# Kernel optimization log

Measured on AMD Instinct MI355X. Metric: run time of the kernel, lower is better.

## Reference

```python
import jax, jax.numpy as jnp
import numpy as np

N_WIRES = 8
DIM = 2 ** N_WIRES  # 256 amplitudes
# PauliZ sign table: Z_SIGNS[w, i] = +1 if bit w of basis index i is 0 else -1
_bits = (np.arange(DIM)[None, :] >> (N_WIRES - 1 - np.arange(N_WIRES))[:, None]) & 1
Z_SIGNS = jnp.asarray(1.0 - 2.0 * _bits, dtype=jnp.float32)  # [8, 256]


def quantum_project(t, theta):
    """Batched 8-wire circuit: RX(x_w) encoder + trainable RX(theta_w) (RX gates on the
    same wire compose additively), then CNOT ring, then <Z_w> for each wire.
    t: [B, S, E] -> returns [B, S, H, 8]."""
    B, S, E = t.shape
    H = E // N_WIRES
    ang = (t.reshape(B, S, H, N_WIRES) + theta) * 0.5  # RX(a)RX(b)=RX(a+b)
    q0 = jnp.cos(ang).astype(jnp.complex64)
    q1 = (-1j * jnp.sin(ang)).astype(jnp.complex64)
    # Build product state |psi> = \otimes_w [cos(a_w/2), -i sin(a_w/2)] -> [B,S,H,256]
    state = jnp.ones((B, S, H, 1), jnp.complex64)
    for w in range(N_WIRES):
        qb = jnp.stack([q0[..., w], q1[..., w]], axis=-1)  # [B,S,H,2]
        state = (state[..., :, None] * qb[..., None, :]).reshape(B, S, H, -1)
    state = state.reshape((B, S, H) + (2,) * N_WIRES)  # wire w on axis 3+w
    # CNOT chain 0->1,...,6->7 then ring-closing 7->0
    for cw, tw in [(w, w + 1) for w in range(N_WIRES - 1)] + [(N_WIRES - 1, 0)]:
        s0 = jax.lax.index_in_dim(state, 0, axis=3 + cw, keepdims=True)
        s1 = jnp.flip(jax.lax.index_in_dim(state, 1, axis=3 + cw, keepdims=True), axis=3 + tw)
        state = jnp.concatenate([s0, s1], axis=3 + cw)
    amps = state.reshape(B, S, H, DIM)
    probs = amps.real * amps.real + amps.imag * amps.imag  # [B,S,H,256] float32
    return jnp.einsum('bshd,wd->bshw', probs, Z_SIGNS)  # <Z_w> per wire


def setup_inputs() -> dict:
    key = jax.random.key(0)
    kx, kq, kk, kv, ko, kt = jax.random.split(key, 6)
    B, S, E = 16, 512, 64
    scale = 1.0 / np.sqrt(E)
    return {
        'x': jax.random.normal(kx, (B, S, E), dtype=jnp.float32),
        'Wq': jax.random.normal(kq, (E, E), dtype=jnp.float32) * scale,
        'Wk': jax.random.normal(kk, (E, E), dtype=jnp.float32) * scale,
        'Wv': jax.random.normal(kv, (E, E), dtype=jnp.float32) * scale,
        'Wo': jax.random.normal(ko, (E, E), dtype=jnp.float32) * scale,
        'theta': jax.random.uniform(kt, (N_WIRES,), dtype=jnp.float32, minval=0.0, maxval=2.0 * np.pi),
    }


def reference(x, Wq, Wk, Wv, Wo, theta):
    B, S, E = x.shape
    q = quantum_project(x @ Wq.T, theta)  # [B,S,H,8]
    k = quantum_project(x @ Wk.T, theta)
    v = quantum_project(x @ Wv.T, theta)
    # NOTE: original code never transposes heads to dim 1, so attention mixes HEADS
    # per token: scores [B,S,H,H]. Faithfully reproduced. d_k = 8.
    scores = jnp.einsum('bsiw,bsjw->bsij', q, k) / jnp.float32(np.sqrt(N_WIRES))
    attn = jax.nn.softmax(scores, axis=-1)  # dropout is identity in eval
    out = jnp.einsum('bsij,bsjw->bsiw', attn, v)  # [B,S,H,8]
    # original: out.transpose(1,2).contiguous().view(B,-1,E) -> scrambled layout
    out = out.transpose(0, 2, 1, 3).reshape(B, -1, E)
    return out @ Wo.T
```

## Files before the change

kernel.cpp:

```cpp
#include <hip/hip_runtime.h>


typedef float  f32x4  __attribute__((ext_vector_type(4)));
typedef short  bf16x8 __attribute__((ext_vector_type(8)));
typedef unsigned short u16;
typedef unsigned int   u32;

#define WRS 72
#define SPS 68

#define DPP_SHR_STEP(d, j, sh)                                                 \
    {                                                                          \
        float _t = __int_as_float(__builtin_amdgcn_update_dpp(                 \
            0x3f800000, __float_as_int(d), 0x110 + sh, 0xf, 0xf, false));      \
        d *= ((j) >= (sh)) ? _t : 1.0f;                                        \
    }

__device__ __forceinline__ u32 bfh(float f) {
    const u32 u = __float_as_uint(f);
    return (u + 0x7FFFu + ((u >> 16) & 1u)) >> 16;
}
__device__ __forceinline__ void bfsplit(float f, u32& h, u32& l) {
    h = bfh(f);
    l = bfh(f - __uint_as_float(h << 16));
}

#define MFMA3(acc, ah, al, bh, bl)                                             \
    acc = __builtin_amdgcn_mfma_f32_16x16x32_bf16(al, bh, acc, 0, 0, 0);       \
    acc = __builtin_amdgcn_mfma_f32_16x16x32_bf16(ah, bl, acc, 0, 0, 0);       \
    acc = __builtin_amdgcn_mfma_f32_16x16x32_bf16(ah, bh, acc, 0, 0, 0);

__global__ __launch_bounds__(512, 1)
void qattn_fused(const float* __restrict__ xg,
                 const float* __restrict__ wqg, const float* __restrict__ wkg,
                 const float* __restrict__ wvg, const float* __restrict__ wog,
                 const float* __restrict__ thg,
                 float* __restrict__ outg)
{
    __shared__ u16 sWh[4 * 64 * WRS];
    __shared__ u16 sWl[4 * 64 * WRS];
    __shared__ u16 sXh[32 * WRS];
    __shared__ u16 sXl[32 * WRS];
    __shared__ __align__(16) float sP[96 * SPS];
    __shared__ u16 sSh[32 * WRS];
    __shared__ u16 sSl[32 * WRS];

    const int tid  = threadIdx.x;
    const int lane = tid & 63;
    const int wg   = tid >> 6;
    const int l15  = lane & 15;
    const int quad = lane >> 4;
    const int j    = lane & 7;
    const int b    = blockIdx.x >> 4;
    const int grp  = blockIdx.x & 15;

    {
        const float* gm[4] = {wqg, wkg, wvg, wog};
        #pragma unroll
        for (int r = 0; r < 8; ++r) {
            const int m   = r >> 1;
            const int idx = (r & 1) * 512 + tid;
            const float4 v = ((const float4*)gm[m])[idx];
            const int e = idx >> 4, c = idx & 15;
            u32 h0, l0, h1, l1, h2, l2, h3, l3;
            bfsplit(v.x, h0, l0); bfsplit(v.y, h1, l1);
            bfsplit(v.z, h2, l2); bfsplit(v.w, h3, l3);
            const int o = (m * 64 + e) * WRS + 4 * c;
            *(uint2*)&sWh[o] = make_uint2(h0 | (h1 << 16), h2 | (h3 << 16));
            *(uint2*)&sWl[o] = make_uint2(l0 | (l1 << 16), l2 | (l3 << 16));
        }
    }
    {
        const float4 v = ((const float4*)(xg + (size_t)(b * 512 + grp * 32) * 64))[tid];
        const int t = tid >> 4, c = tid & 15;
        u32 h0, l0, h1, l1, h2, l2, h3, l3;
        bfsplit(v.x, h0, l0); bfsplit(v.y, h1, l1);
        bfsplit(v.z, h2, l2); bfsplit(v.w, h3, l3);
        const int o = t * WRS + 4 * c;
        *(uint2*)&sXh[o] = make_uint2(h0 | (h1 << 16), h2 | (h3 << 16));
        *(uint2*)&sXl[o] = make_uint2(l0 | (l1 << 16), l2 | (l3 << 16));
    }
    const float thf = thg[j];
    __syncthreads();

    #pragma unroll
    for (int ia = 0; ia < 3; ++ia) {
        const int aid = wg * 3 + ia;
        const int mt = aid & 1, nt = (aid >> 1) & 3, m = aid >> 3;
        const int arow = (mt * 16 + l15) * WRS + quad * 8;
        const int brow = (m * 64 + nt * 16 + l15) * WRS + quad * 8;
        const bf16x8 ah0 = *(const bf16x8*)&sXh[arow];
        const bf16x8 ah1 = *(const bf16x8*)&sXh[arow + 32];
        const bf16x8 al0 = *(const bf16x8*)&sXl[arow];
        const bf16x8 al1 = *(const bf16x8*)&sXl[arow + 32];
        const bf16x8 bh0 = *(const bf16x8*)&sWh[brow];
        const bf16x8 bh1 = *(const bf16x8*)&sWh[brow + 32];
        const bf16x8 bl0 = *(const bf16x8*)&sWl[brow];
        const bf16x8 bl1 = *(const bf16x8*)&sWl[brow + 32];
        f32x4 acc = {0.f, 0.f, 0.f, 0.f};
        MFMA3(acc, ah0, al0, bh0, bl0)
        MFMA3(acc, ah1, al1, bh1, bl1)
        #pragma unroll
        for (int r = 0; r < 4; ++r) {
            const float c = __cosf(acc[r] + thf);
            float d = c;
            DPP_SHR_STEP(d, j, 1)
            DPP_SHR_STEP(d, j, 2)
            DPP_SHR_STEP(d, j, 4)
            float ex = (j == 0) ? 1.0f : c;
            DPP_SHR_STEP(ex, j, 1)
            DPP_SHR_STEP(ex, j, 2)
            DPP_SHR_STEP(ex, j, 4)
            const int row  = m * 32 + mt * 16 + quad * 4 + r;
            const int base = row * SPS + nt * 16 + l15;
            if (j > 0)  sP[base]     = d;
            if (j == 7) sP[base - 7] = ex;
        }
    }
    __syncthreads();

    if (wg < 4) {
        const int tg = wg * 8 + (lane >> 3);
        const int i  = j;
        const int qb = tg * SPS;
        const int kb = (32 + tg) * SPS;
        const int vb = (64 + tg) * SPS;
        float q[8];
        *(float4*)&q[0] = *(const float4*)&sP[qb + 8 * i];
        *(float4*)&q[4] = *(const float4*)&sP[qb + 8 * i + 4];
        float pr[8];
        float sum = 0.f;
        #pragma unroll
        for (int jj = 0; jj < 8; ++jj) {
            const float4 k0 = *(const float4*)&sP[kb + 8 * jj];
            const float4 k1 = *(const float4*)&sP[kb + 8 * jj + 4];
            float s = q[0] * k0.x;
            s = fmaf(q[1], k0.y, s); s = fmaf(q[2], k0.z, s);
            s = fmaf(q[3], k0.w, s); s = fmaf(q[4], k1.x, s);
            s = fmaf(q[5], k1.y, s); s = fmaf(q[6], k1.z, s);
            s = fmaf(q[7], k1.w, s);
            pr[jj] = __expf(s * 0.35355339059327373f);
            sum += pr[jj];
        }
        const float rinv = 1.0f / sum;
        float o[8];
        #pragma unroll
        for (int w = 0; w < 8; ++w) o[w] = 0.f;
        #pragma unroll
        for (int jj = 0; jj < 8; ++jj) {
            const float4 v0 = *(const float4*)&sP[vb + 8 * jj];
            const float4 v1 = *(const float4*)&sP[vb + 8 * jj + 4];
            const float a = pr[jj] * rinv;
            o[0] = fmaf(a, v0.x, o[0]); o[1] = fmaf(a, v0.y, o[1]);
            o[2] = fmaf(a, v0.z, o[2]); o[3] = fmaf(a, v0.w, o[3]);
            o[4] = fmaf(a, v1.x, o[4]); o[5] = fmaf(a, v1.y, o[5]);
            o[6] = fmaf(a, v1.z, o[6]); o[7] = fmaf(a, v1.w, o[7]);
        }
        u32 hh[4], ll[4];
        #pragma unroll
        for (int c = 0; c < 4; ++c) {
            u32 ha, la, hb, lb;
            bfsplit(o[2 * c], ha, la);
            bfsplit(o[2 * c + 1], hb, lb);
            hh[c] = ha | (hb << 16);
            ll[c] = la | (lb << 16);
        }
        const int so = (i * 4 + (tg >> 3)) * WRS + 8 * (tg & 7);
        *(uint4*)&sSh[so] = make_uint4(hh[0], hh[1], hh[2], hh[3]);
        *(uint4*)&sSl[so] = make_uint4(ll[0], ll[1], ll[2], ll[3]);
    }
    __syncthreads();

    {
        const int mt2 = wg >> 2, nt2 = wg & 3;
        const int arow = (mt2 * 16 + l15) * WRS + quad * 8;
        const int brow = (3 * 64 + nt2 * 16 + l15) * WRS + quad * 8;
        const bf16x8 ah0 = *(const bf16x8*)&sSh[arow];
        const bf16x8 ah1 = *(const bf16x8*)&sSh[arow + 32];
        const bf16x8 al0 = *(const bf16x8*)&sSl[arow];
        const bf16x8 al1 = *(const bf16x8*)&sSl[arow + 32];
        const bf16x8 bh0 = *(const bf16x8*)&sWh[brow];
        const bf16x8 bh1 = *(const bf16x8*)&sWh[brow + 32];
        const bf16x8 bl0 = *(const bf16x8*)&sWl[brow];
        const bf16x8 bl1 = *(const bf16x8*)&sWl[brow + 32];
        f32x4 acc = {0.f, 0.f, 0.f, 0.f};
        MFMA3(acc, ah0, al0, bh0, bl0)
        MFMA3(acc, ah1, al1, bh1, bl1)
        const int e = nt2 * 16 + l15;
        #pragma unroll
        for (int r = 0; r < 4; ++r) {
            const int rho = mt2 * 16 + quad * 4 + r;
            const int R   = (rho >> 2) * 64 + grp * 4 + (rho & 3);
            outg[((size_t)(b * 512 + R)) * 64 + e] = acc[r];
        }
    }
}

extern "C" void kernel_launch(void* const* d_in, const int* in_sizes, int n_in,
                              void* d_out, int out_size, void* d_ws, size_t ws_size,
                              hipStream_t stream) {
    const float* x  = (const float*)d_in[0];
    const float* wq = (const float*)d_in[1];
    const float* wk = (const float*)d_in[2];
    const float* wv = (const float*)d_in[3];
    const float* wo = (const float*)d_in[4];
    const float* th = (const float*)d_in[5];
    float* out = (float*)d_out;
    qattn_fused<<<dim3(256), dim3(512), 0, stream>>>(x, wq, wk, wv, wo, th, out);
}
```

Measured before the change: 67.59 us.

## Halve block tile, drop shared weight staging, load weights directly into MFMA registers

Splits the work into 512 blocks of 256 threads handling 16 tokens each instead of 256 blocks of 32 tokens, shrinking shared memory so several blocks fit per CU. Each warp now loads its weight fragments straight from global memory (L2-resident) and converts them to hi/lo bf16 in registers, so the full weight matrices are no longer staged in LDS. It also uses a cheaper hi split that truncates instead of rounding. The cost is redundant weight loads and conversions across blocks and warps, plus some idle lanes in the attention stage.

```diff
diff --git a/kernel.cpp b/kernel.cpp
--- a/kernel.cpp
+++ b/kernel.cpp
@@ -20,9 +20,26 @@
     const u32 u = __float_as_uint(f);
     return (u + 0x7FFFu + ((u >> 16) & 1u)) >> 16;
 }
-__device__ __forceinline__ void bfsplit(float f, u32& h, u32& l) {
-    h = bfh(f);
-    l = bfh(f - __uint_as_float(h << 16));
+__device__ __forceinline__ void bfsplit2(float a, float b, u32& h, u32& l) {
+    const u32 ua = __float_as_uint(a), ub = __float_as_uint(b);
+    h = (ua >> 16) | (ub & 0xFFFF0000u);
+    const float ra = a - __uint_as_float(ua & 0xFFFF0000u);
+    const float rb = b - __uint_as_float(ub & 0xFFFF0000u);
+    l = bfh(ra) | (bfh(rb) << 16);
+}
+__device__ __forceinline__ bf16x8 mk8(u32 a, u32 b, u32 c, u32 d) {
+    uint4 t = make_uint4(a, b, c, d);
+    return *(bf16x8*)&t;
+}
+__device__ __forceinline__ void splitpack(const float4 w0, const float4 w1,
+                                          bf16x8& hi, bf16x8& lo) {
+    u32 h0, l0, h1, l1, h2, l2, h3, l3;
+    bfsplit2(w0.x, w0.y, h0, l0);
+    bfsplit2(w0.z, w0.w, h1, l1);
+    bfsplit2(w1.x, w1.y, h2, l2);
+    bfsplit2(w1.z, w1.w, h3, l3);
+    hi = mk8(h0, h1, h2, h3);
+    lo = mk8(l0, l1, l2, l3);
 }
 
 #define MFMA3(acc, ah, al, bh, bl)                                             \
@@ -30,20 +47,18 @@
     acc = __builtin_amdgcn_mfma_f32_16x16x32_bf16(ah, bl, acc, 0, 0, 0);       \
     acc = __builtin_amdgcn_mfma_f32_16x16x32_bf16(ah, bh, acc, 0, 0, 0);
 
-__global__ __launch_bounds__(512, 1)
+__global__ __launch_bounds__(256, 4)
 void qattn_fused(const float* __restrict__ xg,
                  const float* __restrict__ wqg, const float* __restrict__ wkg,
                  const float* __restrict__ wvg, const float* __restrict__ wog,
                  const float* __restrict__ thg,
                  float* __restrict__ outg)
 {
-    __shared__ u16 sWh[4 * 64 * WRS];
-    __shared__ u16 sWl[4 * 64 * WRS];
-    __shared__ u16 sXh[32 * WRS];
-    __shared__ u16 sXl[32 * WRS];
-    __shared__ __align__(16) float sP[96 * SPS];
-    __shared__ u16 sSh[32 * WRS];
-    __shared__ u16 sSl[32 * WRS];
+    __shared__ u16 sXh[16 * WRS];
+    __shared__ u16 sXl[16 * WRS];
+    __shared__ __align__(16) float sP[48 * SPS];
+    __shared__ u16 sSh[16 * WRS];
+    __shared__ u16 sSl[16 * WRS];
 
     const int tid  = threadIdx.x;
     const int lane = tid & 63;
@@ -51,80 +66,73 @@
     const int l15  = lane & 15;
     const int quad = lane >> 4;
     const int j    = lane & 7;
-    const int b    = blockIdx.x >> 4;
-    const int grp  = blockIdx.x & 15;
-
-    {
-        const float* gm[4] = {wqg, wkg, wvg, wog};
-        #pragma unroll
-        for (int r = 0; r < 8; ++r) {
-            const int m   = r >> 1;
-            const int idx = (r & 1) * 512 + tid;
-            const float4 v = ((const float4*)gm[m])[idx];
-            const int e = idx >> 4, c = idx & 15;
-            u32 h0, l0, h1, l1, h2, l2, h3, l3;
-            bfsplit(v.x, h0, l0); bfsplit(v.y, h1, l1);
-            bfsplit(v.z, h2, l2); bfsplit(v.w, h3, l3);
-            const int o = (m * 64 + e) * WRS + 4 * c;
-            *(uint2*)&sWh[o] = make_uint2(h0 | (h1 << 16), h2 | (h3 << 16));
-            *(uint2*)&sWl[o] = make_uint2(l0 | (l1 << 16), l2 | (l3 << 16));
-        }
-    }
-    {
-        const float4 v = ((const float4*)(xg + (size_t)(b * 512 + grp * 32) * 64))[tid];
-        const int t = tid >> 4, c = tid & 15;
-        u32 h0, l0, h1, l1, h2, l2, h3, l3;
-        bfsplit(v.x, h0, l0); bfsplit(v.y, h1, l1);
-        bfsplit(v.z, h2, l2); bfsplit(v.w, h3, l3);
-        const int o = t * WRS + 4 * c;
-        *(uint2*)&sXh[o] = make_uint2(h0 | (h1 << 16), h2 | (h3 << 16));
-        *(uint2*)&sXl[o] = make_uint2(l0 | (l1 << 16), l2 | (l3 << 16));
+    const int b    = blockIdx.x >> 5;
+    const int grp  = blockIdx.x & 31;
+
+    {
+        const float4 v = ((const float4*)(xg + (size_t)(b * 512 + grp * 16) * 64))[tid];
+        u32 h01, l01, h23, l23;
+        bfsplit2(v.x, v.y, h01, l01);
+        bfsplit2(v.z, v.w, h23, l23);
+        const int o = (tid >> 4) * WRS + 4 * (tid & 15);
+        *(uint2*)&sXh[o] = make_uint2(h01, h23);
+        *(uint2*)&sXl[o] = make_uint2(l01, l23);
     }
     const float thf = thg[j];
     __syncthreads();
 
-    #pragma unroll
-    for (int ia = 0; ia < 3; ++ia) {
-        const int aid = wg * 3 + ia;
-        const int mt = aid & 1, nt = (aid >> 1) & 3, m = aid >> 3;
-        const int arow = (mt * 16 + l15) * WRS + quad * 8;
-        const int brow = (m * 64 + nt * 16 + l15) * WRS + quad * 8;
+    {
+        const int arow = l15 * WRS + quad * 8;
         const bf16x8 ah0 = *(const bf16x8*)&sXh[arow];
         const bf16x8 ah1 = *(const bf16x8*)&sXh[arow + 32];
         const bf16x8 al0 = *(const bf16x8*)&sXl[arow];
         const bf16x8 al1 = *(const bf16x8*)&sXl[arow + 32];
-        const bf16x8 bh0 = *(const bf16x8*)&sWh[brow];
-        const bf16x8 bh1 = *(const bf16x8*)&sWh[brow + 32];
-        const bf16x8 bl0 = *(const bf16x8*)&sWl[brow];
-        const bf16x8 bl1 = *(const bf16x8*)&sWl[brow + 32];
-        f32x4 acc = {0.f, 0.f, 0.f, 0.f};
-        MFMA3(acc, ah0, al0, bh0, bl0)
-        MFMA3(acc, ah1, al1, bh1, bl1)
-        #pragma unroll
-        for (int r = 0; r < 4; ++r) {
-            const float c = __cosf(acc[r] + thf);
-            float d = c;
-            DPP_SHR_STEP(d, j, 1)
-            DPP_SHR_STEP(d, j, 2)
-            DPP_SHR_STEP(d, j, 4)
-            float ex = (j == 0) ? 1.0f : c;
-            DPP_SHR_STEP(ex, j, 1)
-            DPP_SHR_STEP(ex, j, 2)
-            DPP_SHR_STEP(ex, j, 4)
-            const int row  = m * 32 + mt * 16 + quad * 4 + r;
-            const int base = row * SPS + nt * 16 + l15;
-            if (j > 0)  sP[base]     = d;
-            if (j == 7) sP[base - 7] = ex;
+        #pragma unroll
+        for (int ia = 0; ia < 3; ++ia) {
+            const int aid = wg * 3 + ia;
+            const int m = aid >> 2, nt = aid & 3;
+            const float* wm = (m == 0) ? wqg : (m == 1) ? wkg : wvg;
+            const float* wr = wm + (nt * 16 + l15) * 64 + quad * 8;
+            bf16x8 bh0, bl0, bh1, bl1;
+            {
+                const float4 w0 = *(const float4*)wr;
+                const float4 w1 = *(const float4*)(wr + 4);
+                splitpack(w0, w1, bh0, bl0);
+            }
+            {
+                const float4 w0 = *(const float4*)(wr + 32);
+                const float4 w1 = *(const float4*)(wr + 36);
+                splitpack(w0, w1, bh1, bl1);
+            }
+            f32x4 acc = {0.f, 0.f, 0.f, 0.f};
+            MFMA3(acc, ah0, al0, bh0, bl0)
+            MFMA3(acc, ah1, al1, bh1, bl1)
+            #pragma unroll
+            for (int r = 0; r < 4; ++r) {
+                const float c = __cosf(acc[r] + thf);
+                float d = c;
+                DPP_SHR_STEP(d, j, 1)
+                DPP_SHR_STEP(d, j, 2)
+                DPP_SHR_STEP(d, j, 4)
+                float ex = (j == 0) ? 1.0f : c;
+                DPP_SHR_STEP(ex, j, 1)
+                DPP_SHR_STEP(ex, j, 2)
+                DPP_SHR_STEP(ex, j, 4)
+                const int row  = m * 16 + quad * 4 + r;
+                const int base = row * SPS + nt * 16 + l15;
+                if (j > 0)  sP[base]     = d;
+                if (j == 7) sP[base - 7] = ex;
+            }
         }
     }
     __syncthreads();
 
-    if (wg < 4) {
-        const int tg = wg * 8 + (lane >> 3);
+    {
+        const int tg = wg * 4 + (lane >> 4);
         const int i  = j;
         const int qb = tg * SPS;
-        const int kb = (32 + tg) * SPS;
-        const int vb = (64 + tg) * SPS;
+        const int kb = (16 + tg) * SPS;
+        const int vb = (32 + tg) * SPS;
         float q[8];
         *(float4*)&q[0] = *(const float4*)&sP[qb + 8 * i];
         *(float4*)&q[4] = *(const float4*)&sP[qb + 8 * i + 4];
@@ -156,41 +164,44 @@
             o[4] = fmaf(a, v1.x, o[4]); o[5] = fmaf(a, v1.y, o[5]);
             o[6] = fmaf(a, v1.z, o[6]); o[7] = fmaf(a, v1.w, o[7]);
         }
-        u32 hh[4], ll[4];
-        #pragma unroll
-        for (int c = 0; c < 4; ++c) {
-            u32 ha, la, hb, lb;
-            bfsplit(o[2 * c], ha, la);
-            bfsplit(o[2 * c + 1], hb, lb);
-            hh[c] = ha | (hb << 16);
-            ll[c] = la | (lb << 16);
-        }
-        const int so = (i * 4 + (tg >> 3)) * WRS + 8 * (tg & 7);
-        *(uint4*)&sSh[so] = make_uint4(hh[0], hh[1], hh[2], hh[3]);
-        *(uint4*)&sSl[so] = make_uint4(ll[0], ll[1], ll[2], ll[3]);
+        if (!(lane & 8)) {
+            u32 hh[4], ll[4];
+            #pragma unroll
+            for (int c = 0; c < 4; ++c)
+                bfsplit2(o[2 * c], o[2 * c + 1], hh[c], ll[c]);
+            const int so = (i * 2 + (tg >> 3)) * WRS + 8 * (tg & 7);
+            *(uint4*)&sSh[so] = make_uint4(hh[0], hh[1], hh[2], hh[3]);
+            *(uint4*)&sSl[so] = make_uint4(ll[0], ll[1], ll[2], ll[3]);
+        }
     }
     __syncthreads();
 
     {
-        const int mt2 = wg >> 2, nt2 = wg & 3;
-        const int arow = (mt2 * 16 + l15) * WRS + quad * 8;
-        const int brow = (3 * 64 + nt2 * 16 + l15) * WRS + quad * 8;
+        const int arow = l15 * WRS + quad * 8;
         const bf16x8 ah0 = *(const bf16x8*)&sSh[arow];
         const bf16x8 ah1 = *(const bf16x8*)&sSh[arow + 32];
         const bf16x8 al0 = *(const bf16x8*)&sSl[arow];
         const bf16x8 al1 = *(const bf16x8*)&sSl[arow + 32];
-        const bf16x8 bh0 = *(const bf16x8*)&sWh[brow];
-        const bf16x8 bh1 = *(const bf16x8*)&sWh[brow + 32];
-        const bf16x8 bl0 = *(const bf16x8*)&sWl[brow];
-        const bf16x8 bl1 = *(const bf16x8*)&sWl[brow + 32];
+        const float* wr = wog + (wg * 16 + l15) * 64 + quad * 8;
+        bf16x8 bh0, bl0, bh1, bl1;
+        {
+            const float4 w0 = *(const float4*)wr;
+            const float4 w1 = *(const float4*)(wr + 4);
+            splitpack(w0, w1, bh0, bl0);
+        }
+        {
+            const float4 w0 = *(const float4*)(wr + 32);
+            const float4 w1 = *(const float4*)(wr + 36);
+            splitpack(w0, w1, bh1, bl1);
+        }
         f32x4 acc = {0.f, 0.f, 0.f, 0.f};
         MFMA3(acc, ah0, al0, bh0, bl0)
         MFMA3(acc, ah1, al1, bh1, bl1)
-        const int e = nt2 * 16 + l15;
+        const int e = wg * 16 + l15;
         #pragma unroll
         for (int r = 0; r < 4; ++r) {
-            const int rho = mt2 * 16 + quad * 4 + r;
-            const int R   = (rho >> 2) * 64 + grp * 4 + (rho & 3);
+            const int rho = quad * 4 + r;
+            const int R   = (rho >> 1) * 64 + grp * 2 + (rho & 1);
             outg[((size_t)(b * 512 + R)) * 64 + e] = acc[r];
         }
     }
@@ -206,5 +217,5 @@
     const float* wo = (const float*)d_in[4];
     const float* th = (const float*)d_in[5];
     float* out = (float*)d_out;
-    qattn_fused<<<dim3(256), dim3(512), 0, stream>>>(x, wq, wk, wv, wo, th, out);
-}
+    qattn_fused<<<dim3(512), dim3(256), 0, stream>>>(x, wq, wk, wv, wo, th, out);
+}
```

Result: no change. 68.37 us (+1.2%).
